# Kernel tuning notes

Measured on AMD Instinct MI355X. Metric: run time of the kernel, lower is better.

Reference implementation:

```python
import jax, jax.numpy as jnp
import numpy as np

N = 20000      # nodes
E = 320000     # directed edges (before self-loops)
IN, HID, HEADS, OUT = 512, 256, 4, 256
NEG_SLOPE = 0.2  # PyG GATConv default


def setup_inputs() -> dict:
    key = jax.random.key(0)
    ks = jax.random.split(key, 10)
    x = jax.random.normal(ks[0], (N, IN), jnp.float32)
    edge_index = jax.random.randint(ks[1], (2, E), 0, N, jnp.int32)
    W1 = jax.random.normal(ks[2], (IN, HEADS * HID), jnp.float32) / np.sqrt(IN).astype(np.float32)
    att_src1 = jax.random.normal(ks[3], (HEADS, HID), jnp.float32) * 0.1
    att_dst1 = jax.random.normal(ks[4], (HEADS, HID), jnp.float32) * 0.1
    b1 = jnp.zeros((HEADS * HID,), jnp.float32)
    W2 = jax.random.normal(ks[5], (HEADS * HID, OUT), jnp.float32) / np.sqrt(HEADS * HID).astype(np.float32)
    att_src2 = jax.random.normal(ks[6], (1, OUT), jnp.float32) * 0.1
    att_dst2 = jax.random.normal(ks[7], (1, OUT), jnp.float32) * 0.1
    b2 = jnp.zeros((OUT,), jnp.float32)
    return {"x": x, "edge_index": edge_index, "W1": W1, "att_src1": att_src1,
            "att_dst1": att_dst1, "b1": b1, "W2": W2, "att_src2": att_src2,
            "att_dst2": att_dst2, "b2": b2}


def _segment_softmax(logits, seg, num_segments):
    # softmax over edges grouped by destination node (per head)
    m = jax.ops.segment_max(logits, seg, num_segments=num_segments)
    ex = jnp.exp(logits - m[seg])
    s = jax.ops.segment_sum(ex, seg, num_segments=num_segments)
    return ex / (s[seg] + 1e-16)


def _gat_conv(x, src, dst, W, att_src, att_dst, bias, heads, ch, num_nodes, concat):
    # PyG GATConv: h = W x (per head); alpha_e = softmax_dst(LeakyReLU(a_s.h_src + a_d.h_dst))
    h = (x @ W).reshape(num_nodes, heads, ch)          # [N,H,C]
    a_s = (h * att_src).sum(-1)                        # [N,H]
    a_d = (h * att_dst).sum(-1)                        # [N,H]
    logits = jax.nn.leaky_relu(a_s[src] + a_d[dst], NEG_SLOPE)   # [E,H]
    alpha = _segment_softmax(logits, dst, num_nodes)             # [E,H]
    msg = h[src] * alpha[:, :, None]                             # [E,H,C]
    out = jax.ops.segment_sum(msg, dst, num_segments=num_nodes)  # [N,H,C]
    out = out.reshape(num_nodes, heads * ch) if concat else out.mean(axis=1)
    return out + bias


def reference(x, edge_index, W1, att_src1, att_dst1, b1, W2, att_src2, att_dst2, b2):
    # add self-loops (PyG default add_self_loops=True)
    loop = jnp.arange(N, dtype=edge_index.dtype)
    src = jnp.concatenate([edge_index[0], loop])
    dst = jnp.concatenate([edge_index[1], loop])
    h = jax.nn.elu(_gat_conv(x, src, dst, W1, att_src1, att_dst1, b1, HEADS, HID, N, True))
    return _gat_conv(h, src, dst, W2, att_src2, att_dst2, b2, 1, OUT, N, False)
```

## Files before the change

### kernel.cpp

```cpp
#include <hip/hip_runtime.h>
#include <hip/hip_bf16.h>
#include <cfloat>
#include <math.h>

#define N_NODES 20000
#define M_PAD   20096
#define N_EDGES 320000
#define TOT_E   (N_EDGES + N_NODES)
#define EPAD    512
#define IN_F    512
#define HID     256
#define HEADS   4
#define OUT_F   256
#define H1DIM   (HEADS * HID)
#define NEG_SLOPE 0.2f

typedef __attribute__((ext_vector_type(8))) __bf16 bf16x8;
typedef __attribute__((ext_vector_type(4))) __bf16 bf16x4;
typedef __attribute__((ext_vector_type(4))) float f32x4;

__device__ __forceinline__ float lrelu(float x) { return x >= 0.f ? x : NEG_SLOPE * x; }
__device__ __forceinline__ float elu_lite(float x) { return x > 0.f ? x : __expf(x) - 1.f; }

__global__ void k_count(const int* __restrict__ ei, int* __restrict__ deg) {
  int e = blockIdx.x * 256 + threadIdx.x;
  if (e >= TOT_E) return;
  int dst = (e < N_EDGES) ? ei[N_EDGES + e] : (e - N_EDGES);
  atomicAdd(&deg[dst], 1);
}

__global__ void k_scan(const int* __restrict__ deg, int* __restrict__ off) {
  __shared__ int part[256];
  int tid = threadIdx.x;
  const int chunk = (N_NODES + 255) / 256;
  int s0 = tid * chunk;
  int s1 = s0 + chunk; if (s1 > N_NODES) s1 = N_NODES; if (s0 > N_NODES) s0 = N_NODES;
  int s = 0;
  for (int i = s0; i < s1; ++i) s += deg[i];
  part[tid] = s;
  __syncthreads();
  for (int d = 1; d < 256; d <<= 1) {
    int v = (tid >= d) ? part[tid - d] : 0;
    __syncthreads();
    part[tid] += v;
    __syncthreads();
  }
  int run = (tid == 0) ? 0 : part[tid - 1];
  for (int i = s0; i < s1; ++i) { off[i] = run; run += deg[i]; }
  if (tid == 255) off[N_NODES] = run;
}

__global__ void k_fill(const int* __restrict__ ei, const int* __restrict__ off,
                       int* __restrict__ cur, int* __restrict__ csr_src) {
  int e = blockIdx.x * 256 + threadIdx.x;
  if (e >= TOT_E) return;
  int src, dst;
  if (e < N_EDGES) { src = ei[e]; dst = ei[N_EDGES + e]; }
  else             { src = dst = e - N_EDGES; }
  int pos = atomicAdd(&cur[dst], 1);
  csr_src[off[dst] + pos] = src;
}

__global__ void k_f2b(const float* __restrict__ in, __bf16* __restrict__ out, int n4) {
  int i = blockIdx.x * 256 + threadIdx.x;
  if (i >= n4) return;
  float4 v = ((const float4*)in)[i];
  bf16x4 o = { (__bf16)v.x, (__bf16)v.y, (__bf16)v.z, (__bf16)v.w };
  ((bf16x4*)out)[i] = o;
}

__global__ void k_tr_f2b(const float* __restrict__ in, __bf16* __restrict__ out,
                         int R, int Cc) {
  __shared__ float tile[32][33];
  int c0 = blockIdx.x * 32, r0 = blockIdx.y * 32;
  int tx = threadIdx.x & 31, ty = threadIdx.x >> 5;
  for (int rr = ty; rr < 32; rr += 8)
    tile[rr][tx] = in[(size_t)(r0 + rr) * Cc + c0 + tx];
  __syncthreads();
  for (int rr = ty; rr < 32; rr += 8)
    out[(size_t)(c0 + rr) * R + r0 + tx] = (__bf16)tile[tx][rr];
}

__global__ __launch_bounds__(256) void k_gemm_bf16(
    const __bf16* __restrict__ A,
    const __bf16* __restrict__ Bt,
    __bf16* __restrict__ Cb,
    int M, int N, int K)
{
  __shared__ char lds[32768];
  char* As = lds;
  char* Bs = lds + 16384;

  const int t = threadIdx.x;
  const int lane = t & 63;
  const int wid = t >> 6;
  const int wm = wid >> 1, wn = wid & 1;
  const int row0 = blockIdx.y * 128;
  const int col0 = blockIdx.x * 128;

  f32x4 acc[4][4];
#pragma unroll
  for (int i = 0; i < 4; ++i)
#pragma unroll
    for (int j = 0; j < 4; ++j) acc[i][j] = (f32x4){0.f, 0.f, 0.f, 0.f};

  for (int k0 = 0; k0 < K; k0 += 64) {
#pragma unroll
    for (int i = 0; i < 4; ++i) {
      int j = i * 256 + t;
      int r = j >> 3;
      int cc = (j & 7) ^ (r & 7);
      const __bf16* gp = A + (size_t)(row0 + r) * K + k0 + cc * 8;
      __builtin_amdgcn_global_load_lds(
          (const __attribute__((address_space(1))) void*)gp,
          (__attribute__((address_space(3))) void*)(As + j * 16), 16, 0, 0);
    }
#pragma unroll
    for (int i = 0; i < 4; ++i) {
      int j = i * 256 + t;
      int r = j >> 3;
      int cc = (j & 7) ^ (r & 7);
      const __bf16* gp = Bt + (size_t)(col0 + r) * K + k0 + cc * 8;
      __builtin_amdgcn_global_load_lds(
          (const __attribute__((address_space(1))) void*)gp,
          (__attribute__((address_space(3))) void*)(Bs + j * 16), 16, 0, 0);
    }
    __syncthreads();

#pragma unroll
    for (int ks = 0; ks < 2; ++ks) {
      bf16x8 af[4], bfr[4];
#pragma unroll
      for (int i = 0; i < 4; ++i) {
        int rA = wm * 64 + i * 16 + (lane & 15);
        int chA = (ks * 4 + (lane >> 4)) ^ (rA & 7);
        af[i] = *(const bf16x8*)(As + rA * 128 + chA * 16);
        int rB = wn * 64 + i * 16 + (lane & 15);
        int chB = (ks * 4 + (lane >> 4)) ^ (rB & 7);
        bfr[i] = *(const bf16x8*)(Bs + rB * 128 + chB * 16);
      }
#pragma unroll
      for (int i = 0; i < 4; ++i)
#pragma unroll
        for (int jn = 0; jn < 4; ++jn)
          acc[i][jn] = __builtin_amdgcn_mfma_f32_16x16x32_bf16(
              af[i], bfr[jn], acc[i][jn], 0, 0, 0);
    }
    __syncthreads();
  }

#pragma unroll
  for (int i = 0; i < 4; ++i) {
    int growb = row0 + wm * 64 + i * 16 + (lane >> 4) * 4;
#pragma unroll
    for (int jn = 0; jn < 4; ++jn) {
      int gcol = col0 + wn * 64 + jn * 16 + (lane & 15);
#pragma unroll
      for (int r = 0; r < 4; ++r) {
        int grow = growb + r;
        if (grow < M) Cb[(size_t)grow * N + gcol] = (__bf16)acc[i][jn][r];
      }
    }
  }
}

__global__ void k_attn1(const __bf16* __restrict__ h1b, const float* __restrict__ att_s,
                        const float* __restrict__ att_d, float* __restrict__ as,
                        float* __restrict__ ad) {
  int n = blockIdx.x;
  int t = threadIdx.x;
  int head = t >> 6, lane = t & 63;
  bf16x4 hv = *(const bf16x4*)(h1b + (size_t)n * H1DIM + t * 4);
  float4 sv = *(const float4*)(att_s + t * 4);
  float4 dv = *(const float4*)(att_d + t * 4);
  float h0 = (float)hv[0], h1 = (float)hv[1], h2 = (float)hv[2], h3 = (float)hv[3];
  float ss = h0 * sv.x + h1 * sv.y + h2 * sv.z + h3 * sv.w;
  float sd = h0 * dv.x + h1 * dv.y + h2 * dv.z + h3 * dv.w;
#pragma unroll
  for (int d = 32; d; d >>= 1) { ss += __shfl_xor(ss, d); sd += __shfl_xor(sd, d); }
  if (lane == 0) { as[n * HEADS + head] = ss; ad[n * HEADS + head] = sd; }
}

__global__ void k_attn2(const __bf16* __restrict__ h2b, const float* __restrict__ att_s,
                        const float* __restrict__ att_d, float* __restrict__ as,
                        float* __restrict__ ad) {
  int n = blockIdx.x;
  int lane = threadIdx.x;
  bf16x4 hv = *(const bf16x4*)(h2b + (size_t)n * OUT_F + lane * 4);
  float4 sv = *(const float4*)(att_s + lane * 4);
  float4 dv = *(const float4*)(att_d + lane * 4);
  float h0 = (float)hv[0], h1 = (float)hv[1], h2 = (float)hv[2], h3 = (float)hv[3];
  float ss = h0 * sv.x + h1 * sv.y + h2 * sv.z + h3 * sv.w;
  float sd = h0 * dv.x + h1 * dv.y + h2 * dv.z + h3 * dv.w;
#pragma unroll
  for (int d = 32; d; d >>= 1) { ss += __shfl_xor(ss, d); sd += __shfl_xor(sd, d); }
  if (lane == 0) { as[n] = ss; ad[n] = sd; }
}

__global__ void k_w1(const int* __restrict__ off, const int* __restrict__ csr,
                     const float* __restrict__ as, const float* __restrict__ ad,
                     float* __restrict__ wn, float* __restrict__ inv) {
  int n = blockIdx.x;
  int lane = threadIdx.x;
  int beg = off[n], end = off[n + 1];
  float4 adv = *(const float4*)&ad[n * 4];
  float p0 = 0.f, p1 = 0.f, p2 = 0.f, p3 = 0.f;
  for (int p = beg + lane; p < end; p += 64) {
    int s = csr[p];
    float4 av = *(const float4*)&as[s * 4];
    float w0 = __expf(lrelu(av.x + adv.x));
    float w1 = __expf(lrelu(av.y + adv.y));
    float w2 = __expf(lrelu(av.z + adv.z));
    float w3 = __expf(lrelu(av.w + adv.w));
    p0 += w0; p1 += w1; p2 += w2; p3 += w3;
    float4 wv = {w0, w1, w2, w3};
    *(float4*)&wn[(size_t)p * 4] = wv;
  }
#pragma unroll
  for (int d = 32; d; d >>= 1) {
    p0 += __shfl_xor(p0, d); p1 += __shfl_xor(p1, d);
    p2 += __shfl_xor(p2, d); p3 += __shfl_xor(p3, d);
  }
  if (lane == 0) {
    float4 iv = {1.f / (p0 + 1e-16f), 1.f / (p1 + 1e-16f),
                 1.f / (p2 + 1e-16f), 1.f / (p3 + 1e-16f)};
    *(float4*)&inv[n * 4] = iv;
  }
}

__global__ void k_w2(const int* __restrict__ off, const int* __restrict__ csr,
                     const float* __restrict__ as, const float* __restrict__ ad,
                     float* __restrict__ wn, float* __restrict__ inv) {
  int n = blockIdx.x;
  int lane = threadIdx.x;
  int beg = off[n], end = off[n + 1];
  float adv = ad[n];
  float ps = 0.f;
  for (int p = beg + lane; p < end; p += 64) {
    int s = csr[p];
    float w = __expf(lrelu(as[s] + adv));
    wn[p] = w;
    ps += w;
  }
#pragma unroll
  for (int d = 32; d; d >>= 1) ps += __shfl_xor(ps, d);
  if (lane == 0) inv[n] = 1.f / (ps + 1e-16f);
}

__global__ __launch_bounds__(256) void k_gather1(
    const int* __restrict__ off, const int* __restrict__ csr,
    const __bf16* __restrict__ h1b, const float* __restrict__ wn,
    const float* __restrict__ inv, const float* __restrict__ b1,
    __bf16* __restrict__ heluB) {
  int bid = blockIdx.x;
  int slice = bid & 7;
  int head = slice >> 1;
  int cb = slice * 128;
  int w = threadIdx.x >> 6, lane = threadIdx.x & 63;
  int g = lane >> 4;
  int cg = lane & 15;
  int n = (bid >> 3) * 16 + w * 4 + g;
  int beg = off[n], end = off[n + 1];
  int deg = end - beg;
  int itmax = deg;
  itmax = max(itmax, __shfl_xor(itmax, 16));
  itmax = max(itmax, __shfl_xor(itmax, 32));

  float acc[8] = {0.f, 0.f, 0.f, 0.f, 0.f, 0.f, 0.f, 0.f};
  const __bf16* hb = h1b + cb + cg * 8;
#pragma unroll 2
  for (int i = 0; i < itmax; ++i) {
    int e = beg + i;
    int s = csr[e];
    float wv = (i < deg) ? wn[(size_t)e * 4 + head] : 0.f;
    uint4 u = *(const uint4*)(hb + (size_t)s * H1DIM);
    acc[0] = fmaf(wv, __uint_as_float(u.x << 16), acc[0]);
    acc[1] = fmaf(wv, __uint_as_float(u.x & 0xffff0000u), acc[1]);
    acc[2] = fmaf(wv, __uint_as_float(u.y << 16), acc[2]);
    acc[3] = fmaf(wv, __uint_as_float(u.y & 0xffff0000u), acc[3]);
    acc[4] = fmaf(wv, __uint_as_float(u.z << 16), acc[4]);
    acc[5] = fmaf(wv, __uint_as_float(u.z & 0xffff0000u), acc[5]);
    acc[6] = fmaf(wv, __uint_as_float(u.w << 16), acc[6]);
    acc[7] = fmaf(wv, __uint_as_float(u.w & 0xffff0000u), acc[7]);
  }

  float iv = inv[n * 4 + head];
  float4 bv0 = *(const float4*)(b1 + cb + cg * 8);
  float4 bv1 = *(const float4*)(b1 + cb + cg * 8 + 4);
  float bb[8] = {bv0.x, bv0.y, bv0.z, bv0.w, bv1.x, bv1.y, bv1.z, bv1.w};
  bf16x8 o;
#pragma unroll
  for (int k = 0; k < 8; ++k) {
    float v = acc[k] * iv + bb[k];
    o[k] = (__bf16)elu_lite(v);
  }
  *(bf16x8*)(heluB + (size_t)n * H1DIM + cb + cg * 8) = o;
}

__global__ __launch_bounds__(256) void k_gather2(
    const int* __restrict__ off, const int* __restrict__ csr,
    const __bf16* __restrict__ h2b, const float* __restrict__ wn,
    const float* __restrict__ inv, const float* __restrict__ b2,
    float* __restrict__ out) {
  int bid = blockIdx.x;
  int slice = bid & 3;
  int cb = slice * 64;
  int w = threadIdx.x >> 6, lane = threadIdx.x & 63;
  int g = lane >> 3;
  int cg = lane & 7;
  int n = (bid >> 2) * 32 + w * 8 + g;
  int beg = off[n], end = off[n + 1];
  int deg = end - beg;
  int itmax = deg;
  itmax = max(itmax, __shfl_xor(itmax, 8));
  itmax = max(itmax, __shfl_xor(itmax, 16));
  itmax = max(itmax, __shfl_xor(itmax, 32));

  float acc[8] = {0.f, 0.f, 0.f, 0.f, 0.f, 0.f, 0.f, 0.f};
  const __bf16* hb = h2b + cb + cg * 8;
#pragma unroll 2
  for (int i = 0; i < itmax; ++i) {
    int e = beg + i;
    int s = csr[e];
    float wv = (i < deg) ? wn[e] : 0.f;
    uint4 u = *(const uint4*)(hb + (size_t)s * OUT_F);
    acc[0] = fmaf(wv, __uint_as_float(u.x << 16), acc[0]);
    acc[1] = fmaf(wv, __uint_as_float(u.x & 0xffff0000u), acc[1]);
    acc[2] = fmaf(wv, __uint_as_float(u.y << 16), acc[2]);
    acc[3] = fmaf(wv, __uint_as_float(u.y & 0xffff0000u), acc[3]);
    acc[4] = fmaf(wv, __uint_as_float(u.z << 16), acc[4]);
    acc[5] = fmaf(wv, __uint_as_float(u.z & 0xffff0000u), acc[5]);
    acc[6] = fmaf(wv, __uint_as_float(u.w << 16), acc[6]);
    acc[7] = fmaf(wv, __uint_as_float(u.w & 0xffff0000u), acc[7]);
  }

  float iv = inv[n];
  float4 bv0 = *(const float4*)(b2 + cb + cg * 8);
  float4 bv1 = *(const float4*)(b2 + cb + cg * 8 + 4);
  float* op = out + (size_t)n * OUT_F + cb + cg * 8;
  float4 o0 = {acc[0] * iv + bv0.x, acc[1] * iv + bv0.y,
               acc[2] * iv + bv0.z, acc[3] * iv + bv0.w};
  float4 o1 = {acc[4] * iv + bv1.x, acc[5] * iv + bv1.y,
               acc[6] * iv + bv1.z, acc[7] * iv + bv1.w};
  *(float4*)op = o0;
  *(float4*)(op + 4) = o1;
}

extern "C" void kernel_launch(void* const* d_in, const int* in_sizes, int n_in,
                              void* d_out, int out_size, void* d_ws, size_t ws_size,
                              hipStream_t stream) {
  const float* x      = (const float*)d_in[0];
  const int*   ei     = (const int*)d_in[1];
  const float* W1     = (const float*)d_in[2];
  const float* att_s1 = (const float*)d_in[3];
  const float* att_d1 = (const float*)d_in[4];
  const float* b1     = (const float*)d_in[5];
  const float* W2     = (const float*)d_in[6];
  const float* att_s2 = (const float*)d_in[7];
  const float* att_d2 = (const float*)d_in[8];
  const float* b2     = (const float*)d_in[9];
  float* out = (float*)d_out;

  char* w = (char*)d_ws;
  auto alloc = [&](size_t bytes) {
    char* p = w;
    w += (bytes + 255) & ~(size_t)255;
    return p;
  };
  int*    deg   = (int*)alloc((size_t)N_NODES * 4);
  int*    off   = (int*)alloc((size_t)(N_NODES + 1) * 4);
  int*    cur   = (int*)alloc((size_t)N_NODES * 4);
  int*    csr   = (int*)alloc((size_t)(TOT_E + EPAD) * 4);
  float*  as1   = (float*)alloc((size_t)N_NODES * HEADS * 4);
  float*  ad1   = (float*)alloc((size_t)N_NODES * HEADS * 4);
  float*  as2   = (float*)alloc((size_t)N_NODES * 4);
  float*  ad2   = (float*)alloc((size_t)N_NODES * 4);
  float*  wn1   = (float*)alloc((size_t)(TOT_E + EPAD) * HEADS * 4);
  float*  inv1  = (float*)alloc((size_t)N_NODES * HEADS * 4);
  float*  wn2   = (float*)alloc((size_t)(TOT_E + EPAD) * 4);
  float*  inv2  = (float*)alloc((size_t)N_NODES * 4);
  __bf16* xb    = (__bf16*)alloc((size_t)M_PAD * IN_F * 2);
  __bf16* w1t   = (__bf16*)alloc((size_t)H1DIM * IN_F * 2);
  __bf16* w2t   = (__bf16*)alloc((size_t)OUT_F * H1DIM * 2);
  __bf16* h1b   = (__bf16*)alloc((size_t)M_PAD * H1DIM * 2);
  __bf16* heluB = (__bf16*)alloc((size_t)M_PAD * H1DIM * 2);
  __bf16* h2b   = (__bf16*)alloc((size_t)M_PAD * OUT_F * 2);
  if ((size_t)(w - (char*)d_ws) > ws_size) return;

  hipMemsetAsync(deg, 0, (size_t)N_NODES * 4, stream);
  hipMemsetAsync(cur, 0, (size_t)N_NODES * 4, stream);
  hipMemsetAsync(csr + TOT_E, 0, (size_t)EPAD * 4, stream);

  k_count<<<(TOT_E + 255) / 256, 256, 0, stream>>>(ei, deg);
  k_scan<<<1, 256, 0, stream>>>(deg, off);
  k_fill<<<(TOT_E + 255) / 256, 256, 0, stream>>>(ei, off, cur, csr);

  int n4 = N_NODES * IN_F / 4;
  k_f2b<<<(n4 + 255) / 256, 256, 0, stream>>>(x, xb, n4);
  k_tr_f2b<<<dim3(H1DIM / 32, IN_F / 32), 256, 0, stream>>>(W1, w1t, IN_F, H1DIM);
  k_tr_f2b<<<dim3(OUT_F / 32, H1DIM / 32), 256, 0, stream>>>(W2, w2t, H1DIM, OUT_F);

  k_gemm_bf16<<<dim3(H1DIM / 128, M_PAD / 128), 256, 0, stream>>>(
      xb, w1t, h1b, N_NODES, H1DIM, IN_F);
  k_attn1<<<N_NODES, 256, 0, stream>>>(h1b, att_s1, att_d1, as1, ad1);
  k_w1<<<N_NODES, 64, 0, stream>>>(off, csr, as1, ad1, wn1, inv1);
  k_gather1<<<(N_NODES / 16) * 8, 256, 0, stream>>>(off, csr, h1b, wn1, inv1, b1, heluB);

  k_gemm_bf16<<<dim3(OUT_F / 128, M_PAD / 128), 256, 0, stream>>>(
      heluB, w2t, h2b, N_NODES, OUT_F, H1DIM);
  k_attn2<<<N_NODES, 64, 0, stream>>>(h2b, att_s2, att_d2, as2, ad2);
  k_w2<<<N_NODES, 64, 0, stream>>>(off, csr, as2, ad2, wn2, inv2);
  k_gather2<<<(N_NODES / 32) * 4, 256, 0, stream>>>(off, csr, h2b, wn2, inv2, b2, out);
}
```

Before: 307.3 us.

## Degree-sort nodes for gathers, software-pipeline neighbor loads, reshape gather1 tiling

Adds a counting sort that buckets nodes by in-degree into a permutation, and both gather kernels now process nodes in that order. Nodes in a wavefront then have similar degrees, which cuts the idle lanes caused by looping to the group's maximum degree. The gather loops also prefetch the next neighbor's row and weight one iteration ahead. gather1 is remapped to 8 nodes per wave with 64-column slices in two phases. The cost is three small extra kernels plus two memsets, scattered output writes, and less locality in the writes to heluB and out.

```diff
diff --git a/kernel.cpp b/kernel.cpp
--- a/kernel.cpp
+++ b/kernel.cpp
@@ -59,6 +59,37 @@
   else             { src = dst = e - N_EDGES; }
   int pos = atomicAdd(&cur[dst], 1);
   csr_src[off[dst] + pos] = src;
+}
+
+__global__ void k_hist(const int* __restrict__ off, int* __restrict__ hist) {
+  int n = blockIdx.x * 256 + threadIdx.x;
+  if (n >= N_NODES) return;
+  int d = off[n + 1] - off[n];
+  atomicAdd(&hist[min(d, 255)], 1);
+}
+
+__global__ void k_hscan(const int* __restrict__ hist, int* __restrict__ hoff) {
+  __shared__ int sh[256];
+  int t = threadIdx.x;
+  int v = hist[t];
+  sh[t] = v;
+  __syncthreads();
+  for (int d = 1; d < 256; d <<= 1) {
+    int x = (t >= d) ? sh[t - d] : 0;
+    __syncthreads();
+    sh[t] += x;
+    __syncthreads();
+  }
+  hoff[t] = sh[t] - v;
+}
+
+__global__ void k_perm(const int* __restrict__ off, const int* __restrict__ hoff,
+                       int* __restrict__ cur2, int* __restrict__ perm) {
+  int n = blockIdx.x * 256 + threadIdx.x;
+  if (n >= N_NODES) return;
+  int b = min(off[n + 1] - off[n], 255);
+  int pos = atomicAdd(&cur2[b], 1);
+  perm[hoff[b] + pos] = n;
 }
 
 __global__ void k_f2b(const float* __restrict__ in, __bf16* __restrict__ out, int n4) {
@@ -249,66 +280,20 @@
 
 __global__ __launch_bounds__(256) void k_gather1(
     const int* __restrict__ off, const int* __restrict__ csr,
-    const __bf16* __restrict__ h1b, const float* __restrict__ wn,
-    const float* __restrict__ inv, const float* __restrict__ b1,
-    __bf16* __restrict__ heluB) {
+    const int* __restrict__ perm, const __bf16* __restrict__ h1b,
+    const float* __restrict__ wn, const float* __restrict__ inv,
+    const float* __restrict__ b1, __bf16* __restrict__ heluB) {
   int bid = blockIdx.x;
-  int slice = bid & 7;
-  int head = slice >> 1;
-  int cb = slice * 128;
-  int w = threadIdx.x >> 6, lane = threadIdx.x & 63;
-  int g = lane >> 4;
-  int cg = lane & 15;
-  int n = (bid >> 3) * 16 + w * 4 + g;
-  int beg = off[n], end = off[n + 1];
-  int deg = end - beg;
-  int itmax = deg;
-  itmax = max(itmax, __shfl_xor(itmax, 16));
-  itmax = max(itmax, __shfl_xor(itmax, 32));
-
-  float acc[8] = {0.f, 0.f, 0.f, 0.f, 0.f, 0.f, 0.f, 0.f};
-  const __bf16* hb = h1b + cb + cg * 8;
-#pragma unroll 2
-  for (int i = 0; i < itmax; ++i) {
-    int e = beg + i;
-    int s = csr[e];
-    float wv = (i < deg) ? wn[(size_t)e * 4 + head] : 0.f;
-    uint4 u = *(const uint4*)(hb + (size_t)s * H1DIM);
-    acc[0] = fmaf(wv, __uint_as_float(u.x << 16), acc[0]);
-    acc[1] = fmaf(wv, __uint_as_float(u.x & 0xffff0000u), acc[1]);
-    acc[2] = fmaf(wv, __uint_as_float(u.y << 16), acc[2]);
-    acc[3] = fmaf(wv, __uint_as_float(u.y & 0xffff0000u), acc[3]);
-    acc[4] = fmaf(wv, __uint_as_float(u.z << 16), acc[4]);
-    acc[5] = fmaf(wv, __uint_as_float(u.z & 0xffff0000u), acc[5]);
-    acc[6] = fmaf(wv, __uint_as_float(u.w << 16), acc[6]);
-    acc[7] = fmaf(wv, __uint_as_float(u.w & 0xffff0000u), acc[7]);
-  }
-
-  float iv = inv[n * 4 + head];
-  float4 bv0 = *(const float4*)(b1 + cb + cg * 8);
-  float4 bv1 = *(const float4*)(b1 + cb + cg * 8 + 4);
-  float bb[8] = {bv0.x, bv0.y, bv0.z, bv0.w, bv1.x, bv1.y, bv1.z, bv1.w};
-  bf16x8 o;
-#pragma unroll
-  for (int k = 0; k < 8; ++k) {
-    float v = acc[k] * iv + bb[k];
-    o[k] = (__bf16)elu_lite(v);
-  }
-  *(bf16x8*)(heluB + (size_t)n * H1DIM + cb + cg * 8) = o;
-}
-
-__global__ __launch_bounds__(256) void k_gather2(
-    const int* __restrict__ off, const int* __restrict__ csr,
-    const __bf16* __restrict__ h2b, const float* __restrict__ wn,
-    const float* __restrict__ inv, const float* __restrict__ b2,
-    float* __restrict__ out) {
-  int bid = blockIdx.x;
-  int slice = bid & 3;
+  int phase = (bid >= 5000) ? 1 : 0;
+  int r = bid - phase * 5000;
+  int slice = (r & 7) | (phase << 3);
+  int grp = r >> 3;
   int cb = slice * 64;
+  int head = slice >> 2;
   int w = threadIdx.x >> 6, lane = threadIdx.x & 63;
   int g = lane >> 3;
   int cg = lane & 7;
-  int n = (bid >> 2) * 32 + w * 8 + g;
+  int n = perm[grp * 32 + w * 8 + g];
   int beg = off[n], end = off[n + 1];
   int deg = end - beg;
   int itmax = deg;
@@ -317,21 +302,82 @@
   itmax = max(itmax, __shfl_xor(itmax, 32));
 
   float acc[8] = {0.f, 0.f, 0.f, 0.f, 0.f, 0.f, 0.f, 0.f};
+  const __bf16* hb = h1b + cb + cg * 8;
+
+  int s0 = csr[beg];
+  float w0 = wn[(size_t)beg * 4 + head];
+  uint4 u0 = *(const uint4*)(hb + (size_t)s0 * H1DIM);
+  for (int i = 0; i < itmax; ++i) {
+    bool v = (i + 1 < deg);
+    int e1 = beg + i + 1;
+    int s1 = v ? csr[e1] : 0;
+    float w1 = v ? wn[(size_t)e1 * 4 + head] : 0.f;
+    uint4 u1 = *(const uint4*)(hb + (size_t)s1 * H1DIM);
+    acc[0] = fmaf(w0, __uint_as_float(u0.x << 16), acc[0]);
+    acc[1] = fmaf(w0, __uint_as_float(u0.x & 0xffff0000u), acc[1]);
+    acc[2] = fmaf(w0, __uint_as_float(u0.y << 16), acc[2]);
+    acc[3] = fmaf(w0, __uint_as_float(u0.y & 0xffff0000u), acc[3]);
+    acc[4] = fmaf(w0, __uint_as_float(u0.z << 16), acc[4]);
+    acc[5] = fmaf(w0, __uint_as_float(u0.z & 0xffff0000u), acc[5]);
+    acc[6] = fmaf(w0, __uint_as_float(u0.w << 16), acc[6]);
+    acc[7] = fmaf(w0, __uint_as_float(u0.w & 0xffff0000u), acc[7]);
+    u0 = u1; w0 = w1;
+  }
+
+  float iv = inv[n * 4 + head];
+  float4 bv0 = *(const float4*)(b1 + cb + cg * 8);
+  float4 bv1 = *(const float4*)(b1 + cb + cg * 8 + 4);
+  float bb[8] = {bv0.x, bv0.y, bv0.z, bv0.w, bv1.x, bv1.y, bv1.z, bv1.w};
+  bf16x8 o;
+#pragma unroll
+  for (int k = 0; k < 8; ++k) {
+    float v = acc[k] * iv + bb[k];
+    o[k] = (__bf16)elu_lite(v);
+  }
+  *(bf16x8*)(heluB + (size_t)n * H1DIM + cb + cg * 8) = o;
+}
+
+__global__ __launch_bounds__(256) void k_gather2(
+    const int* __restrict__ off, const int* __restrict__ csr,
+    const int* __restrict__ perm, const __bf16* __restrict__ h2b,
+    const float* __restrict__ wn, const float* __restrict__ inv,
+    const float* __restrict__ b2, float* __restrict__ out) {
+  int bid = blockIdx.x;
+  int slice = bid & 3;
+  int grp = bid >> 2;
+  int cb = slice * 64;
+  int w = threadIdx.x >> 6, lane = threadIdx.x & 63;
+  int g = lane >> 3;
+  int cg = lane & 7;
+  int n = perm[grp * 32 + w * 8 + g];
+  int beg = off[n], end = off[n + 1];
+  int deg = end - beg;
+  int itmax = deg;
+  itmax = max(itmax, __shfl_xor(itmax, 8));
+  itmax = max(itmax, __shfl_xor(itmax, 16));
+  itmax = max(itmax, __shfl_xor(itmax, 32));
+
+  float acc[8] = {0.f, 0.f, 0.f, 0.f, 0.f, 0.f, 0.f, 0.f};
   const __bf16* hb = h2b + cb + cg * 8;
-#pragma unroll 2
+
+  int s0 = csr[beg];
+  float w0 = wn[beg];
+  uint4 u0 = *(const uint4*)(hb + (size_t)s0 * OUT_F);
   for (int i = 0; i < itmax; ++i) {
-    int e = beg + i;
-    int s = csr[e];
-    float wv = (i < deg) ? wn[e] : 0.f;
-    uint4 u = *(const uint4*)(hb + (size_t)s * OUT_F);
-    acc[0] = fmaf(wv, __uint_as_float(u.x << 16), acc[0]);
-    acc[1] = fmaf(wv, __uint_as_float(u.x & 0xffff0000u), acc[1]);
-    acc[2] = fmaf(wv, __uint_as_float(u.y << 16), acc[2]);
-    acc[3] = fmaf(wv, __uint_as_float(u.y & 0xffff0000u), acc[3]);
-    acc[4] = fmaf(wv, __uint_as_float(u.z << 16), acc[4]);
-    acc[5] = fmaf(wv, __uint_as_float(u.z & 0xffff0000u), acc[5]);
-    acc[6] = fmaf(wv, __uint_as_float(u.w << 16), acc[6]);
-    acc[7] = fmaf(wv, __uint_as_float(u.w & 0xffff0000u), acc[7]);
+    bool v = (i + 1 < deg);
+    int e1 = beg + i + 1;
+    int s1 = v ? csr[e1] : 0;
+    float w1 = v ? wn[e1] : 0.f;
+    uint4 u1 = *(const uint4*)(hb + (size_t)s1 * OUT_F);
+    acc[0] = fmaf(w0, __uint_as_float(u0.x << 16), acc[0]);
+    acc[1] = fmaf(w0, __uint_as_float(u0.x & 0xffff0000u), acc[1]);
+    acc[2] = fmaf(w0, __uint_as_float(u0.y << 16), acc[2]);
+    acc[3] = fmaf(w0, __uint_as_float(u0.y & 0xffff0000u), acc[3]);
+    acc[4] = fmaf(w0, __uint_as_float(u0.z << 16), acc[4]);
+    acc[5] = fmaf(w0, __uint_as_float(u0.z & 0xffff0000u), acc[5]);
+    acc[6] = fmaf(w0, __uint_as_float(u0.w << 16), acc[6]);
+    acc[7] = fmaf(w0, __uint_as_float(u0.w & 0xffff0000u), acc[7]);
+    u0 = u1; w0 = w1;
   }
 
   float iv = inv[n];
@@ -371,6 +417,10 @@
   int*    off   = (int*)alloc((size_t)(N_NODES + 1) * 4);
   int*    cur   = (int*)alloc((size_t)N_NODES * 4);
   int*    csr   = (int*)alloc((size_t)(TOT_E + EPAD) * 4);
+  int*    hist  = (int*)alloc(256 * 4);
+  int*    hoff  = (int*)alloc(256 * 4);
+  int*    cur2  = (int*)alloc(256 * 4);
+  int*    perm  = (int*)alloc((size_t)N_NODES * 4);
   float*  as1   = (float*)alloc((size_t)N_NODES * HEADS * 4);
   float*  ad1   = (float*)alloc((size_t)N_NODES * HEADS * 4);
   float*  as2   = (float*)alloc((size_t)N_NODES * 4);
@@ -390,10 +440,15 @@
   hipMemsetAsync(deg, 0, (size_t)N_NODES * 4, stream);
   hipMemsetAsync(cur, 0, (size_t)N_NODES * 4, stream);
   hipMemsetAsync(csr + TOT_E, 0, (size_t)EPAD * 4, stream);
+  hipMemsetAsync(hist, 0, 256 * 4, stream);
+  hipMemsetAsync(cur2, 0, 256 * 4, stream);
 
   k_count<<<(TOT_E + 255) / 256, 256, 0, stream>>>(ei, deg);
   k_scan<<<1, 256, 0, stream>>>(deg, off);
   k_fill<<<(TOT_E + 255) / 256, 256, 0, stream>>>(ei, off, cur, csr);
+  k_hist<<<(N_NODES + 255) / 256, 256, 0, stream>>>(off, hist);
+  k_hscan<<<1, 256, 0, stream>>>(hist, hoff);
+  k_perm<<<(N_NODES + 255) / 256, 256, 0, stream>>>(off, hoff, cur2, perm);
 
   int n4 = N_NODES * IN_F / 4;
   k_f2b<<<(n4 + 255) / 256, 256, 0, stream>>>(x, xb, n4);
@@ -404,11 +459,11 @@
       xb, w1t, h1b, N_NODES, H1DIM, IN_F);
   k_attn1<<<N_NODES, 256, 0, stream>>>(h1b, att_s1, att_d1, as1, ad1);
   k_w1<<<N_NODES, 64, 0, stream>>>(off, csr, as1, ad1, wn1, inv1);
-  k_gather1<<<(N_NODES / 16) * 8, 256, 0, stream>>>(off, csr, h1b, wn1, inv1, b1, heluB);
+  k_gather1<<<10000, 256, 0, stream>>>(off, csr, perm, h1b, wn1, inv1, b1, heluB);
 
   k_gemm_bf16<<<dim3(OUT_F / 128, M_PAD / 128), 256, 0, stream>>>(
       heluB, w2t, h2b, N_NODES, OUT_F, H1DIM);
   k_attn2<<<N_NODES, 64, 0, stream>>>(h2b, att_s2, att_d2, as2, ad2);
   k_w2<<<N_NODES, 64, 0, stream>>>(off, csr, as2, ad2, wn2, inv2);
-  k_gather2<<<(N_NODES / 32) * 4, 256, 0, stream>>>(off, csr, h2b, wn2, inv2, b2, out);
-}
+  k_gather2<<<2500, 256, 0, stream>>>(off, csr, perm, h2b, wn2, inv2, b2, out);
+}
```

Result: slower. 459.1 us (+49.4%).
